# Performance work log

Measured on AMD Instinct MI355X. Metric: run time of the kernel, lower is better.

## Reference

```python
import jax, jax.numpy as jnp
import numpy as np

D_MODEL, N_HEADS, N_KV, HEAD_DIM, D_LAT = 1024, 8, 2, 128, 32
N_REP = N_HEADS // N_KV  # 4
B, T = 2, 2048


def setup_inputs() -> dict:
    key = jax.random.key(0)
    ks = jax.random.split(key, 8)
    s = lambda fan_in: 1.0 / np.sqrt(fan_in)
    return {
        "x": jax.random.normal(ks[0], (B, T, D_MODEL), jnp.float32),
        # weights stored as [in, out] (transpose of torch Linear.weight)
        "wq": jax.random.normal(ks[1], (D_MODEL, N_HEADS * HEAD_DIM), jnp.float32) * s(D_MODEL),
        "wk_down": jax.random.normal(ks[2], (D_MODEL, N_KV * D_LAT), jnp.float32) * s(D_MODEL),
        "wv_down": jax.random.normal(ks[3], (D_MODEL, N_KV * D_LAT), jnp.float32) * s(D_MODEL),
        "wk_up": jax.random.normal(ks[4], (D_LAT, HEAD_DIM), jnp.float32) * s(D_LAT),
        "wv_up": jax.random.normal(ks[5], (D_LAT, HEAD_DIM), jnp.float32) * s(D_LAT),
        "wo": jax.random.normal(ks[6], (N_HEADS * HEAD_DIM, D_MODEL), jnp.float32) * s(N_HEADS * HEAD_DIM),
    }


def reference(x, wq, wk_down, wv_down, wk_up, wv_up, wo):
    Bq, Tq, _ = x.shape
    scale = HEAD_DIM ** -0.5  # SDPA default scale
    # Q: [B,T,Hkv,Rep,Dh] (grouped view avoids materializing repeated K/V)
    q = (x @ wq).reshape(Bq, Tq, N_KV, N_REP, HEAD_DIM)
    # latent KV: [B,T,Hkv,Dl] -> up-project to [B,T,Hkv,Dh]
    k_lat = (x @ wk_down).reshape(Bq, Tq, N_KV, D_LAT)
    v_lat = (x @ wv_down).reshape(Bq, Tq, N_KV, D_LAT)
    k = jnp.einsum("bkhl,ld->bkhd", k_lat, wk_up)
    v = jnp.einsum("bkhl,ld->bkhd", v_lat, wv_up)
    # causal attention, GQA via grouped einsum (no repeat_interleave copy)
    scores = jnp.einsum("bqhrd,bkhd->bhrqk", q, k) * scale  # [B,Hkv,Rep,T,T]
    causal = jnp.tril(jnp.ones((Tq, Tq), dtype=bool))
    scores = jnp.where(causal, scores, jnp.finfo(scores.dtype).min)
    probs = jax.nn.softmax(scores, axis=-1)
    y = jnp.einsum("bhrqk,bkhd->bqhrd", probs, v)  # [B,T,Hkv,Rep,Dh]
    y = y.reshape(Bq, Tq, N_HEADS * HEAD_DIM)
    return y @ wo
```

## Files before the change

### kernel.cpp

```cpp
#include <hip/hip_runtime.h>
#include <hip/hip_bf16.h>


typedef __bf16 bf16_t;
typedef bf16_t bf16x8 __attribute__((ext_vector_type(8)));
typedef float f32x4 __attribute__((ext_vector_type(4)));

__device__ inline bf16x8 cvt8(const float* __restrict__ p) {
  f32x4 a = *(const f32x4*)p, b = *(const f32x4*)(p + 4);
  bf16x8 r;
#pragma unroll
  for (int i = 0; i < 4; ++i) { r[i] = (bf16_t)a[i]; r[4 + i] = (bf16_t)b[i]; }
  return r;
}

__global__ void prep_fused(const float* __restrict__ wq, const float* __restrict__ wkd,
                           const float* __restrict__ wvd, const float* __restrict__ wku,
                           const float* __restrict__ wvu, const float* __restrict__ wo,
                           float* __restrict__ Wqkv_nat, float* __restrict__ Wcomb_nat) {
  const int tid = threadIdx.x;
  if (blockIdx.x < 1024) {
    const int c = blockIdx.x;
    __shared__ float wkuT[128][33];
    {
      const int l = tid >> 3, d0 = (tid & 7) * 16;
      const float* wp = wku + l * 128 + d0;
#pragma unroll
      for (int q = 0; q < 4; ++q) {
        f32x4 w = *(const f32x4*)(wp + q * 4);
#pragma unroll
        for (int i = 0; i < 4; ++i) wkuT[d0 + q * 4 + i][l] = w[i];
      }
    }
    __syncthreads();
    const int h = tid >> 5, l = tid & 31;
    const float* wqp = wq + c * 1024 + h * 128;
    float acc = 0.f;
#pragma unroll
    for (int d = 0; d < 128; ++d) acc += wqp[d] * wkuT[d][l];
    Wqkv_nat[c * 384 + tid] = acc;
    if (tid < 128)
      Wqkv_nat[c * 384 + 256 + tid] = (tid < 64) ? wkd[c * 64 + tid] : wvd[c * 64 + tid - 64];
  } else {
    const int b2 = blockIdx.x - 1024;
    const int rc = b2 >> 2, m = (b2 & 3) * 256 + tid;
    const int h = rc >> 5, l = rc & 31;
    const float* wvup = wvu + l * 128;
    const float* wop = wo + (size_t)h * 128 * 1024 + m;
    float acc = 0.f;
#pragma unroll
    for (int d = 0; d < 128; ++d) acc += wvup[d] * wop[(size_t)d * 1024];
    Wcomb_nat[rc * 1024 + m] = acc;
  }
}

__global__ void transpose_fused(const float* __restrict__ inq, bf16_t* __restrict__ outq,
                                const float* __restrict__ inc, bf16_t* __restrict__ outc) {
  __shared__ float t[32][33];
  const float* in; bf16_t* out; int R, tx, ty;
  if (blockIdx.x < 384) { in = inq; out = outq; R = 1024; tx = blockIdx.x % 12; ty = blockIdx.x / 12; }
  else { int r = blockIdx.x - 384; in = inc; out = outc; R = 256; tx = r % 32; ty = r / 32; }
  const int C = (blockIdx.x < 384) ? 384 : 1024;
  const int bx = tx * 32, by = ty * 32;
  const int x = threadIdx.x, y0 = threadIdx.y;
#pragma unroll
  for (int i = 0; i < 32; i += 8)
    t[y0 + i][x] = in[(size_t)(by + y0 + i) * C + bx + x];
  __syncthreads();
#pragma unroll
  for (int i = 0; i < 32; i += 8)
    out[(size_t)(bx + y0 + i) * R + by + x] = (bf16_t)t[x][y0 + i];
}

__global__ __launch_bounds__(256) void gemm_qkv(
    const float* __restrict__ A, const bf16_t* __restrict__ Bt,
    bf16_t* __restrict__ C) {
  __shared__ bf16_t As[64][72];
  __shared__ bf16_t Bs[128][72];
  const int tid = threadIdx.x;
  const int wave = tid >> 6, lane = tid & 63;
  const int quad = lane >> 4, col = lane & 15;
  const int wm = (wave >> 1) * 32, wn = (wave & 1) * 64;
  const int m0 = blockIdx.y * 64, n0 = blockIdx.x * 128;

  f32x4 acc[2][4];
#pragma unroll
  for (int i = 0; i < 2; ++i)
#pragma unroll
    for (int j = 0; j < 4; ++j) acc[i][j] = (f32x4){0.f, 0.f, 0.f, 0.f};

  const int ar = tid >> 2, ac = (tid & 3) * 16;
  const int br = tid >> 1, bc = (tid & 1) * 32;
  const float* aP = A + (size_t)(m0 + ar) * 1024 + ac;
  const bf16_t* bP = Bt + (size_t)(n0 + br) * 1024 + bc;

  bf16x8 aR0 = cvt8(aP), aR1 = cvt8(aP + 8);
  bf16x8 bR0 = *(const bf16x8*)bP, bR1 = *(const bf16x8*)(bP + 8);
  bf16x8 bR2 = *(const bf16x8*)(bP + 16), bR3 = *(const bf16x8*)(bP + 24);

  for (int kt = 0; kt < 16; ++kt) {
    *(bf16x8*)&As[ar][ac] = aR0; *(bf16x8*)&As[ar][ac + 8] = aR1;
    *(bf16x8*)&Bs[br][bc] = bR0; *(bf16x8*)&Bs[br][bc + 8] = bR1;
    *(bf16x8*)&Bs[br][bc + 16] = bR2; *(bf16x8*)&Bs[br][bc + 24] = bR3;
    __syncthreads();
    if (kt < 15) {
      const int k0 = (kt + 1) * 64;
      aR0 = cvt8(aP + k0); aR1 = cvt8(aP + k0 + 8);
      bR0 = *(const bf16x8*)(bP + k0); bR1 = *(const bf16x8*)(bP + k0 + 8);
      bR2 = *(const bf16x8*)(bP + k0 + 16); bR3 = *(const bf16x8*)(bP + k0 + 24);
    }
#pragma unroll
    for (int ks = 0; ks < 2; ++ks) {
      bf16x8 af[2], bfr[4];
#pragma unroll
      for (int i = 0; i < 2; ++i) af[i] = *(const bf16x8*)&As[wm + i * 16 + col][ks * 32 + quad * 8];
#pragma unroll
      for (int j = 0; j < 4; ++j) bfr[j] = *(const bf16x8*)&Bs[wn + j * 16 + col][ks * 32 + quad * 8];
#pragma unroll
      for (int i = 0; i < 2; ++i)
#pragma unroll
        for (int j = 0; j < 4; ++j)
          acc[i][j] = __builtin_amdgcn_mfma_f32_16x16x32_bf16(af[i], bfr[j], acc[i][j], 0, 0, 0);
    }
    __syncthreads();
  }

#pragma unroll
  for (int i = 0; i < 2; ++i) {
    const int rg = m0 + wm + i * 16 + quad * 4;
#pragma unroll
    for (int j = 0; j < 4; ++j) {
      const int cg = n0 + wn + j * 16 + col;
#pragma unroll
      for (int v = 0; v < 4; ++v)
        C[(size_t)(rg + v) * 384 + cg] = (bf16_t)acc[i][j][v];
    }
  }
}

__global__ __launch_bounds__(256) void gemm_out(
    const bf16_t* __restrict__ A, const bf16_t* __restrict__ Bt,
    float* __restrict__ C) {
  __shared__ bf16_t As[128][72];
  __shared__ bf16_t Bs[128][72];
  const int tid = threadIdx.x;
  const int wave = tid >> 6, lane = tid & 63;
  const int quad = lane >> 4, col = lane & 15;
  const int wm = (wave >> 1) * 64, wn = (wave & 1) * 64;
  const int m0 = blockIdx.y * 128, n0 = blockIdx.x * 128;

  f32x4 acc[4][4];
#pragma unroll
  for (int i = 0; i < 4; ++i)
#pragma unroll
    for (int j = 0; j < 4; ++j) acc[i][j] = (f32x4){0.f, 0.f, 0.f, 0.f};

  const int ar = tid >> 1, ac = (tid & 1) * 32;
  const bf16_t* aP = A + (size_t)(m0 + ar) * 384 + ac;
  const bf16_t* bP = Bt + (size_t)(n0 + ar) * 256 + ac;

  bf16x8 aR0 = *(const bf16x8*)aP, aR1 = *(const bf16x8*)(aP + 8);
  bf16x8 aR2 = *(const bf16x8*)(aP + 16), aR3 = *(const bf16x8*)(aP + 24);
  bf16x8 bR0 = *(const bf16x8*)bP, bR1 = *(const bf16x8*)(bP + 8);
  bf16x8 bR2 = *(const bf16x8*)(bP + 16), bR3 = *(const bf16x8*)(bP + 24);

  for (int kt = 0; kt < 4; ++kt) {
    *(bf16x8*)&As[ar][ac] = aR0; *(bf16x8*)&As[ar][ac + 8] = aR1;
    *(bf16x8*)&As[ar][ac + 16] = aR2; *(bf16x8*)&As[ar][ac + 24] = aR3;
    *(bf16x8*)&Bs[ar][ac] = bR0; *(bf16x8*)&Bs[ar][ac + 8] = bR1;
    *(bf16x8*)&Bs[ar][ac + 16] = bR2; *(bf16x8*)&Bs[ar][ac + 24] = bR3;
    __syncthreads();
    if (kt < 3) {
      const int k0 = (kt + 1) * 64;
      aR0 = *(const bf16x8*)(aP + k0); aR1 = *(const bf16x8*)(aP + k0 + 8);
      aR2 = *(const bf16x8*)(aP + k0 + 16); aR3 = *(const bf16x8*)(aP + k0 + 24);
      bR0 = *(const bf16x8*)(bP + k0); bR1 = *(const bf16x8*)(bP + k0 + 8);
      bR2 = *(const bf16x8*)(bP + k0 + 16); bR3 = *(const bf16x8*)(bP + k0 + 24);
    }
#pragma unroll
    for (int ks = 0; ks < 2; ++ks) {
      bf16x8 af[4], bfr[4];
#pragma unroll
      for (int i = 0; i < 4; ++i) af[i] = *(const bf16x8*)&As[wm + i * 16 + col][ks * 32 + quad * 8];
#pragma unroll
      for (int j = 0; j < 4; ++j) bfr[j] = *(const bf16x8*)&Bs[wn + j * 16 + col][ks * 32 + quad * 8];
#pragma unroll
      for (int i = 0; i < 4; ++i)
#pragma unroll
        for (int j = 0; j < 4; ++j)
          acc[i][j] = __builtin_amdgcn_mfma_f32_16x16x32_bf16(af[i], bfr[j], acc[i][j], 0, 0, 0);
    }
    __syncthreads();
  }

#pragma unroll
  for (int i = 0; i < 4; ++i) {
    const int rg = m0 + wm + i * 16 + quad * 4;
#pragma unroll
    for (int j = 0; j < 4; ++j) {
      const int cg = n0 + wn + j * 16 + col;
#pragma unroll
      for (int v = 0; v < 4; ++v)
        C[(size_t)(rg + v) * 1024 + cg] = acc[i][j][v];
    }
  }
}

__global__ __launch_bounds__(256) void attn_lat(bf16_t* QKV) {
  const int bi = blockIdx.x;
  const int half = bi >> 8, rest = bi & 255;
  const int qt = half ? 127 - (rest >> 1) : (rest >> 1);
  const int hkv = rest & 1, b = half;
  const int tid = threadIdx.x;
  const int wave = tid >> 6, lane = tid & 63;
  const int quad = lane >> 4, col = lane & 15;

  __shared__ bf16_t Ks[128][40];
  __shared__ bf16_t Vt[32][136];
  __shared__ bf16_t Ps[4][16][136];

  const int qb = qt * 16;
  const size_t rowbase = (size_t)b * 2048;
  const int qcol0 = (hkv * 4 + wave) * 32;

  bf16x8 a_q = *(const bf16x8*)(QKV + (rowbase + qb + col) * 384 + qcol0 + quad * 8);

  f32x4 o0 = (f32x4){0.f, 0.f, 0.f, 0.f};
  f32x4 o1 = (f32x4){0.f, 0.f, 0.f, 0.f};
  float lsum[4] = {0.f, 0.f, 0.f, 0.f};

  const int nkt = (qb >> 7) + 1;
  const float scale = 0.08838834764831843f;

  const int kr = tid >> 1, dc = (tid & 1) * 16;
  const bf16_t* kvBase = QKV + (rowbase + kr) * 384 + 256 + hkv * 32 + dc;
  bf16x8 kA = *(const bf16x8*)kvBase, kB = *(const bf16x8*)(kvBase + 8);
  bf16x8 vA = *(const bf16x8*)(kvBase + 64), vB = *(const bf16x8*)(kvBase + 72);

  for (int kt = 0; kt < nkt; ++kt) {
    const int kb = kt * 128;
    *(bf16x8*)&Ks[kr][dc] = kA;
    *(bf16x8*)&Ks[kr][dc + 8] = kB;
#pragma unroll
    for (int t = 0; t < 8; ++t) { Vt[dc + t][kr] = vA[t]; Vt[dc + 8 + t][kr] = vB[t]; }
    __syncthreads();
    if (kt + 1 < nkt) {
      const bf16_t* np = kvBase + (size_t)(kt + 1) * 128 * 384;
      kA = *(const bf16x8*)np; kB = *(const bf16x8*)(np + 8);
      vA = *(const bf16x8*)(np + 64); vB = *(const bf16x8*)(np + 72);
    }

    f32x4 s[8];
#pragma unroll
    for (int k8 = 0; k8 < 8; ++k8) {
      bf16x8 bk = *(const bf16x8*)&Ks[k8 * 16 + col][quad * 8];
      s[k8] = __builtin_amdgcn_mfma_f32_16x16x32_bf16(a_q, bk, (f32x4){0.f, 0.f, 0.f, 0.f}, 0, 0, 0);
    }

    const bool full = (kb + 128 <= qb);
#pragma unroll
    for (int v = 0; v < 4; ++v) {
      const int qr = quad * 4 + v;
      const int qg = qb + qr;
#pragma unroll
      for (int k8 = 0; k8 < 8; ++k8) {
        float xx = s[k8][v] * scale;
        if (!full && (kb + k8 * 16 + col > qg)) xx = -1e30f;
        const float p = __expf(xx);
        lsum[v] += p;
        Ps[wave][qr][k8 * 16 + col] = (bf16_t)p;
      }
    }
    __syncthreads();

#pragma unroll
    for (int kc = 0; kc < 4; ++kc) {
      bf16x8 a_p = *(const bf16x8*)&Ps[wave][col][kc * 32 + quad * 8];
      bf16x8 bv0 = *(const bf16x8*)&Vt[col][kc * 32 + quad * 8];
      bf16x8 bv1 = *(const bf16x8*)&Vt[16 + col][kc * 32 + quad * 8];
      o0 = __builtin_amdgcn_mfma_f32_16x16x32_bf16(a_p, bv0, o0, 0, 0, 0);
      o1 = __builtin_amdgcn_mfma_f32_16x16x32_bf16(a_p, bv1, o1, 0, 0, 0);
    }
    __syncthreads();
  }

#pragma unroll
  for (int v = 0; v < 4; ++v) {
    float l = lsum[v];
#pragma unroll
    for (int off = 8; off; off >>= 1) l += __shfl_xor(l, off, 64);
    const float inv = 1.f / l;
    const size_t r = (rowbase + qb + quad * 4 + v) * 384 + qcol0;
    QKV[r + col] = (bf16_t)(o0[v] * inv);
    QKV[r + 16 + col] = (bf16_t)(o1[v] * inv);
  }
}

extern "C" void kernel_launch(void* const* d_in, const int* in_sizes, int n_in,
                              void* d_out, int out_size, void* d_ws, size_t ws_size,
                              hipStream_t stream) {
  (void)in_sizes; (void)n_in; (void)out_size; (void)ws_size;
  const float* x   = (const float*)d_in[0];
  const float* wq  = (const float*)d_in[1];
  const float* wkd = (const float*)d_in[2];
  const float* wvd = (const float*)d_in[3];
  const float* wku = (const float*)d_in[4];
  const float* wvu = (const float*)d_in[5];
  const float* wo  = (const float*)d_in[6];
  float* out = (float*)d_out;

  float* Wqkv_nat  = (float*)d_ws;
  float* Wcomb_nat = Wqkv_nat + (size_t)1024 * 384;
  bf16_t* WqkvT  = (bf16_t*)(Wcomb_nat + (size_t)256 * 1024);
  bf16_t* WcombT = WqkvT + (size_t)384 * 1024;
  bf16_t* QKV    = WcombT + (size_t)1024 * 256;

  prep_fused<<<2048, 256, 0, stream>>>(wq, wkd, wvd, wku, wvu, wo, Wqkv_nat, Wcomb_nat);
  transpose_fused<<<640, dim3(32, 8), 0, stream>>>(Wqkv_nat, WqkvT, Wcomb_nat, WcombT);

  gemm_qkv<<<dim3(3, 64), 256, 0, stream>>>(x, WqkvT, QKV);
  attn_lat<<<512, 256, 0, stream>>>(QKV);
  gemm_out<<<dim3(8, 32), 256, 0, stream>>>(QKV, WcombT, out);
}
```

Before: 165.7 us.

## Fuse weight prep into one MFMA kernel and double-buffer attention K/V tiles

Replaces the scalar FP32 weight-folding kernel and the separate transpose kernel with one kernel. That kernel computes the folded weights with bf16 MFMA and writes the transposed bf16 layouts directly. This removes one launch and the FP32 intermediate round trip, but the folded weights now go through bf16 inputs, which reduces precision. In attention, K/V tiles are double-buffered in LDS and the barrier between the softmax writes and the PV MFMA becomes a compiler fence, leaving one barrier per tile. That fence is safe only because Ps is private to each wave.

After: 139.8 us. -15.6%, faster.

```diff
diff --git a/kernel.cpp b/kernel.cpp
--- a/kernel.cpp
+++ b/kernel.cpp
@@ -14,62 +14,108 @@
   return r;
 }
 
-__global__ void prep_fused(const float* __restrict__ wq, const float* __restrict__ wkd,
-                           const float* __restrict__ wvd, const float* __restrict__ wku,
-                           const float* __restrict__ wvu, const float* __restrict__ wo,
-                           float* __restrict__ Wqkv_nat, float* __restrict__ Wcomb_nat) {
+__global__ __launch_bounds__(256) void prep_mfma(
+    const float* __restrict__ wq, const float* __restrict__ wkd,
+    const float* __restrict__ wvd, const float* __restrict__ wku,
+    const float* __restrict__ wvu, const float* __restrict__ wo,
+    bf16_t* __restrict__ WqkvT, bf16_t* __restrict__ WcombT) {
+  __shared__ __align__(16) char smem[34816];
   const int tid = threadIdx.x;
-  if (blockIdx.x < 1024) {
-    const int c = blockIdx.x;
-    __shared__ float wkuT[128][33];
+  const int wave = tid >> 6, lane = tid & 63;
+  const int quad = lane >> 4, col = lane & 15;
+  const int bi = blockIdx.x;
+
+  if (bi < 64) {
+    const int h = bi >> 3;
+    const int c0 = (bi & 7) * 128 + wave * 32;
+    f32x4 acc[2][2];
+#pragma unroll
+    for (int i = 0; i < 2; ++i)
+#pragma unroll
+      for (int j = 0; j < 2; ++j) acc[i][j] = (f32x4){0.f, 0.f, 0.f, 0.f};
+#pragma unroll
+    for (int ks = 0; ks < 4; ++ks) {
+      const int ko = ks * 32 + quad * 8;
+      bf16x8 a0 = cvt8(wku + col * 128 + ko);
+      bf16x8 a1 = cvt8(wku + (16 + col) * 128 + ko);
+      bf16x8 b0 = cvt8(wq + (size_t)(c0 + col) * 1024 + h * 128 + ko);
+      bf16x8 b1 = cvt8(wq + (size_t)(c0 + 16 + col) * 1024 + h * 128 + ko);
+      acc[0][0] = __builtin_amdgcn_mfma_f32_16x16x32_bf16(a0, b0, acc[0][0], 0, 0, 0);
+      acc[0][1] = __builtin_amdgcn_mfma_f32_16x16x32_bf16(a0, b1, acc[0][1], 0, 0, 0);
+      acc[1][0] = __builtin_amdgcn_mfma_f32_16x16x32_bf16(a1, b0, acc[1][0], 0, 0, 0);
+      acc[1][1] = __builtin_amdgcn_mfma_f32_16x16x32_bf16(a1, b1, acc[1][1], 0, 0, 0);
+    }
+#pragma unroll
+    for (int ms = 0; ms < 2; ++ms)
+#pragma unroll
+      for (int ns = 0; ns < 2; ++ns)
+#pragma unroll
+        for (int v = 0; v < 4; ++v)
+          WqkvT[(size_t)(h * 32 + ms * 16 + quad * 4 + v) * 1024 + c0 + ns * 16 + col] =
+              (bf16_t)acc[ms][ns][v];
+  } else if (bi < 128) {
+    const int b2 = bi - 64;
+    const int h = b2 >> 3, m0 = (b2 & 7) * 128;
+    bf16_t(*B_lds)[136] = (bf16_t(*)[136])smem;
     {
-      const int l = tid >> 3, d0 = (tid & 7) * 16;
-      const float* wp = wku + l * 128 + d0;
+      const int d = tid >> 1, mh = (tid & 1) * 64;
+      const float* wp = wo + (size_t)(h * 128 + d) * 1024 + m0 + mh;
+#pragma unroll
+      for (int i = 0; i < 16; ++i) {
+        f32x4 w4 = *(const f32x4*)(wp + i * 4);
+#pragma unroll
+        for (int t = 0; t < 4; ++t) B_lds[mh + i * 4 + t][d] = (bf16_t)w4[t];
+      }
+    }
+    __syncthreads();
+    f32x4 acc[2][2];
+#pragma unroll
+    for (int i = 0; i < 2; ++i)
+#pragma unroll
+      for (int j = 0; j < 2; ++j) acc[i][j] = (f32x4){0.f, 0.f, 0.f, 0.f};
+#pragma unroll
+    for (int ks = 0; ks < 4; ++ks) {
+      const int ko = ks * 32 + quad * 8;
+      bf16x8 a0 = cvt8(wvu + col * 128 + ko);
+      bf16x8 a1 = cvt8(wvu + (16 + col) * 128 + ko);
+      bf16x8 b0 = *(const bf16x8*)&B_lds[wave * 32 + col][ko];
+      bf16x8 b1 = *(const bf16x8*)&B_lds[wave * 32 + 16 + col][ko];
+      acc[0][0] = __builtin_amdgcn_mfma_f32_16x16x32_bf16(a0, b0, acc[0][0], 0, 0, 0);
+      acc[0][1] = __builtin_amdgcn_mfma_f32_16x16x32_bf16(a0, b1, acc[0][1], 0, 0, 0);
+      acc[1][0] = __builtin_amdgcn_mfma_f32_16x16x32_bf16(a1, b0, acc[1][0], 0, 0, 0);
+      acc[1][1] = __builtin_amdgcn_mfma_f32_16x16x32_bf16(a1, b1, acc[1][1], 0, 0, 0);
+    }
+#pragma unroll
+    for (int ms = 0; ms < 2; ++ms)
+#pragma unroll
+      for (int ns = 0; ns < 2; ++ns)
+#pragma unroll
+        for (int v = 0; v < 4; ++v)
+          WcombT[(size_t)(m0 + wave * 32 + ns * 16 + col) * 256 +
+                 h * 32 + ms * 16 + quad * 4 + v] = (bf16_t)acc[ms][ns][v];
+  } else {
+    const int b3 = bi - 128;
+    const int mat = b3 >> 4, c0 = (b3 & 15) * 64;
+    const float* in = mat ? wvd : wkd;
+    bf16_t(*tT)[72] = (bf16_t(*)[72])smem;
+    {
+      const int cc = tid >> 2, jq = (tid & 3) * 16;
+      const float* ip = in + (size_t)(c0 + cc) * 64 + jq;
 #pragma unroll
       for (int q = 0; q < 4; ++q) {
-        f32x4 w = *(const f32x4*)(wp + q * 4);
-#pragma unroll
-        for (int i = 0; i < 4; ++i) wkuT[d0 + q * 4 + i][l] = w[i];
+        f32x4 v4 = *(const f32x4*)(ip + q * 4);
+#pragma unroll
+        for (int t = 0; t < 4; ++t) tT[jq + q * 4 + t][cc] = (bf16_t)v4[t];
       }
     }
     __syncthreads();
-    const int h = tid >> 5, l = tid & 31;
-    const float* wqp = wq + c * 1024 + h * 128;
-    float acc = 0.f;
-#pragma unroll
-    for (int d = 0; d < 128; ++d) acc += wqp[d] * wkuT[d][l];
-    Wqkv_nat[c * 384 + tid] = acc;
-    if (tid < 128)
-      Wqkv_nat[c * 384 + 256 + tid] = (tid < 64) ? wkd[c * 64 + tid] : wvd[c * 64 + tid - 64];
-  } else {
-    const int b2 = blockIdx.x - 1024;
-    const int rc = b2 >> 2, m = (b2 & 3) * 256 + tid;
-    const int h = rc >> 5, l = rc & 31;
-    const float* wvup = wvu + l * 128;
-    const float* wop = wo + (size_t)h * 128 * 1024 + m;
-    float acc = 0.f;
-#pragma unroll
-    for (int d = 0; d < 128; ++d) acc += wvup[d] * wop[(size_t)d * 1024];
-    Wcomb_nat[rc * 1024 + m] = acc;
-  }
-}
-
-__global__ void transpose_fused(const float* __restrict__ inq, bf16_t* __restrict__ outq,
-                                const float* __restrict__ inc, bf16_t* __restrict__ outc) {
-  __shared__ float t[32][33];
-  const float* in; bf16_t* out; int R, tx, ty;
-  if (blockIdx.x < 384) { in = inq; out = outq; R = 1024; tx = blockIdx.x % 12; ty = blockIdx.x / 12; }
-  else { int r = blockIdx.x - 384; in = inc; out = outc; R = 256; tx = r % 32; ty = r / 32; }
-  const int C = (blockIdx.x < 384) ? 384 : 1024;
-  const int bx = tx * 32, by = ty * 32;
-  const int x = threadIdx.x, y0 = threadIdx.y;
-#pragma unroll
-  for (int i = 0; i < 32; i += 8)
-    t[y0 + i][x] = in[(size_t)(by + y0 + i) * C + bx + x];
-  __syncthreads();
-#pragma unroll
-  for (int i = 0; i < 32; i += 8)
-    out[(size_t)(bx + y0 + i) * R + by + x] = (bf16_t)t[x][y0 + i];
+    {
+      const int j = tid >> 2, cq = (tid & 3) * 16;
+      bf16_t* op = WqkvT + (size_t)(256 + mat * 64 + j) * 1024 + c0 + cq;
+      *(bf16x8*)op = *(const bf16x8*)&tT[j][cq];
+      *(bf16x8*)(op + 8) = *(const bf16x8*)&tT[j][cq + 8];
+    }
+  }
 }
 
 __global__ __launch_bounds__(256) void gemm_qkv(
@@ -215,8 +261,8 @@
   const int wave = tid >> 6, lane = tid & 63;
   const int quad = lane >> 4, col = lane & 15;
 
-  __shared__ bf16_t Ks[128][40];
-  __shared__ bf16_t Vt[32][136];
+  __shared__ bf16_t Ks[2][128][40];
+  __shared__ bf16_t Vt[2][32][136];
   __shared__ bf16_t Ps[4][16][136];
 
   const int qb = qt * 16;
@@ -234,17 +280,24 @@
 
   const int kr = tid >> 1, dc = (tid & 1) * 16;
   const bf16_t* kvBase = QKV + (rowbase + kr) * 384 + 256 + hkv * 32 + dc;
-  bf16x8 kA = *(const bf16x8*)kvBase, kB = *(const bf16x8*)(kvBase + 8);
-  bf16x8 vA = *(const bf16x8*)(kvBase + 64), vB = *(const bf16x8*)(kvBase + 72);
+
+  {
+    bf16x8 kA = *(const bf16x8*)kvBase, kB = *(const bf16x8*)(kvBase + 8);
+    bf16x8 vA = *(const bf16x8*)(kvBase + 64), vB = *(const bf16x8*)(kvBase + 72);
+    *(bf16x8*)&Ks[0][kr][dc] = kA;
+    *(bf16x8*)&Ks[0][kr][dc + 8] = kB;
+#pragma unroll
+    for (int t = 0; t < 8; ++t) { Vt[0][dc + t][kr] = vA[t]; Vt[0][dc + 8 + t][kr] = vB[t]; }
+  }
+  __syncthreads();
 
   for (int kt = 0; kt < nkt; ++kt) {
+    const int cur = kt & 1;
     const int kb = kt * 128;
-    *(bf16x8*)&Ks[kr][dc] = kA;
-    *(bf16x8*)&Ks[kr][dc + 8] = kB;
-#pragma unroll
-    for (int t = 0; t < 8; ++t) { Vt[dc + t][kr] = vA[t]; Vt[dc + 8 + t][kr] = vB[t]; }
-    __syncthreads();
-    if (kt + 1 < nkt) {
+    const bool more = (kt + 1 < nkt);
+
+    bf16x8 kA, kB, vA, vB;
+    if (more) {
       const bf16_t* np = kvBase + (size_t)(kt + 1) * 128 * 384;
       kA = *(const bf16x8*)np; kB = *(const bf16x8*)(np + 8);
       vA = *(const bf16x8*)(np + 64); vB = *(const bf16x8*)(np + 72);
@@ -253,7 +306,7 @@
     f32x4 s[8];
 #pragma unroll
     for (int k8 = 0; k8 < 8; ++k8) {
-      bf16x8 bk = *(const bf16x8*)&Ks[k8 * 16 + col][quad * 8];
+      bf16x8 bk = *(const bf16x8*)&Ks[cur][k8 * 16 + col][quad * 8];
       s[k8] = __builtin_amdgcn_mfma_f32_16x16x32_bf16(a_q, bk, (f32x4){0.f, 0.f, 0.f, 0.f}, 0, 0, 0);
     }
 
@@ -271,15 +324,22 @@
         Ps[wave][qr][k8 * 16 + col] = (bf16_t)p;
       }
     }
-    __syncthreads();
+    __asm__ __volatile__("" ::: "memory");
 
 #pragma unroll
     for (int kc = 0; kc < 4; ++kc) {
       bf16x8 a_p = *(const bf16x8*)&Ps[wave][col][kc * 32 + quad * 8];
-      bf16x8 bv0 = *(const bf16x8*)&Vt[col][kc * 32 + quad * 8];
-      bf16x8 bv1 = *(const bf16x8*)&Vt[16 + col][kc * 32 + quad * 8];
+      bf16x8 bv0 = *(const bf16x8*)&Vt[cur][col][kc * 32 + quad * 8];
+      bf16x8 bv1 = *(const bf16x8*)&Vt[cur][16 + col][kc * 32 + quad * 8];
       o0 = __builtin_amdgcn_mfma_f32_16x16x32_bf16(a_p, bv0, o0, 0, 0, 0);
       o1 = __builtin_amdgcn_mfma_f32_16x16x32_bf16(a_p, bv1, o1, 0, 0, 0);
+    }
+
+    if (more) {
+      *(bf16x8*)&Ks[cur ^ 1][kr][dc] = kA;
+      *(bf16x8*)&Ks[cur ^ 1][kr][dc + 8] = kB;
+#pragma unroll
+      for (int t = 0; t < 8; ++t) { Vt[cur ^ 1][dc + t][kr] = vA[t]; Vt[cur ^ 1][dc + 8 + t][kr] = vB[t]; }
     }
     __syncthreads();
   }
@@ -309,15 +369,11 @@
   const float* wo  = (const float*)d_in[6];
   float* out = (float*)d_out;
 
-  float* Wqkv_nat  = (float*)d_ws;
-  float* Wcomb_nat = Wqkv_nat + (size_t)1024 * 384;
-  bf16_t* WqkvT  = (bf16_t*)(Wcomb_nat + (size_t)256 * 1024);
+  bf16_t* WqkvT  = (bf16_t*)d_ws;
   bf16_t* WcombT = WqkvT + (size_t)384 * 1024;
   bf16_t* QKV    = WcombT + (size_t)1024 * 256;
 
-  prep_fused<<<2048, 256, 0, stream>>>(wq, wkd, wvd, wku, wvu, wo, Wqkv_nat, Wcomb_nat);
-  transpose_fused<<<640, dim3(32, 8), 0, stream>>>(Wqkv_nat, WqkvT, Wcomb_nat, WcombT);
-
+  prep_mfma<<<160, 256, 0, stream>>>(wq, wkd, wvd, wku, wvu, wo, WqkvT, WcombT);
   gemm_qkv<<<dim3(3, 64), 256, 0, stream>>>(x, WqkvT, QKV);
   attn_lat<<<512, 256, 0, stream>>>(QKV);
   gemm_out<<<dim3(8, 32), 256, 0, stream>>>(QKV, WcombT, out);
```
